# Kernel optimization log

Measured on AMD Instinct MI355X. Metric: run time of the kernel, lower is better.

The kernel has to match this reference:

```python
import jax, jax.numpy as jnp
import numpy as np

N_NODES = 50000
N_EDGES = 1_600_000
IN_DIM = 256
OUT_DIM = 128
NEG_SLOPE = 0.01  # F.leaky_relu default


def setup_inputs() -> dict:
    key = jax.random.key(0)
    k1, k2, k3, k4, k5 = jax.random.split(key, 5)
    x = jax.random.normal(k1, (N_NODES, IN_DIM), dtype=jnp.float32)
    # glorot_init: uniform in [-r, r], r = sqrt(6/(in+out))
    r = np.sqrt(6.0 / (IN_DIM + OUT_DIM)).astype(np.float32)
    weight = jax.random.uniform(k2, (IN_DIM, OUT_DIM), dtype=jnp.float32, minval=-r, maxval=r)
    adj_rows = jax.random.randint(k3, (N_EDGES,), 0, N_NODES, dtype=jnp.int64 if jax.config.jax_enable_x64 else jnp.int32)
    adj_cols = jax.random.randint(k4, (N_EDGES,), 0, N_NODES, dtype=jnp.int64 if jax.config.jax_enable_x64 else jnp.int32)
    adj_vals = jax.random.uniform(k5, (N_EDGES,), dtype=jnp.float32)
    return {"x": x, "weight": weight, "adj_vals": adj_vals,
            "adj_rows": adj_rows, "adj_cols": adj_cols}


def reference(x, weight, adj_vals, adj_rows, adj_cols):
    # h = X @ W : [N, OUT_DIM]
    h = x @ weight
    # sparse adj @ h via edge-list SpMM: out[r] += v * h[c]
    msgs = adj_vals[:, None] * h[adj_cols]            # [E, OUT_DIM]
    agg = jax.ops.segment_sum(msgs, adj_rows, num_segments=N_NODES)
    # leaky_relu epilogue
    return jnp.where(agg >= 0, agg, NEG_SLOPE * agg)
```

## Files before the change

kernel.cpp:

```cpp
#include <hip/hip_runtime.h>
#include <hip/hip_fp16.h>

#define N_NODES 50000
#define N_EDGES 1600000
#define IN_DIM 256
#define OUT_DIM 128
#define NEG_SLOPE 0.01f

#define BIN_SH    5
#define BIN_ROWS  32
#define NBIN      ((N_NODES + BIN_ROWS - 1) / BIN_ROWS)
#define CAPB      1280
#define OVF_CAP   65536

#define SCAT_BLOCKS 256
#define CONVW_BLOCKS 8
#define EPB_S (N_EDGES / SCAT_BLOCKS)
#define SCAT_ITERS ((EPB_S + 511) / 512)

typedef _Float16 f16x8 __attribute__((ext_vector_type(8)));
typedef float    f32x4 __attribute__((ext_vector_type(4)));
typedef float    f32x8 __attribute__((ext_vector_type(8)));

__device__ __forceinline__ float lrelu(float v) {
    return v >= 0.f ? v : NEG_SLOPE * v;
}

#define BM 128
#define GEMM_BLOCKS ((N_NODES + BM - 1) / BM)

#define CVT16(lo, hi) do { \
    lo[0]=(_Float16)xr[0].x; lo[1]=(_Float16)xr[0].y; lo[2]=(_Float16)xr[0].z; lo[3]=(_Float16)xr[0].w; \
    lo[4]=(_Float16)xr[1].x; lo[5]=(_Float16)xr[1].y; lo[6]=(_Float16)xr[1].z; lo[7]=(_Float16)xr[1].w; \
    hi[0]=(_Float16)xr[2].x; hi[1]=(_Float16)xr[2].y; hi[2]=(_Float16)xr[2].z; hi[3]=(_Float16)xr[2].w; \
    hi[4]=(_Float16)xr[3].x; hi[5]=(_Float16)xr[3].y; hi[6]=(_Float16)xr[3].z; hi[7]=(_Float16)xr[3].w; \
} while (0)

__global__ __launch_bounds__(256, 2) void gemm_xw_mfma(const float* __restrict__ x,
                                                       const __half* __restrict__ wtl,
                                                       __half* __restrict__ h) {
    __shared__ f16x8 wt8[32 * 128];
    __shared__ f16x8 xs8[2][4][BM];

    const int t    = threadIdx.x;
    const int lane = t & 63;
    const int wv   = t >> 6;
    const int row0 = blockIdx.x * BM;

    {
        const int4* src = (const int4*)wtl;
        int4* dst = (int4*)wt8;
#pragma unroll
        for (int i = 0; i < 16; ++i) dst[i * 256 + t] = src[i * 256 + t];
    }

    const int srow = t >> 1;
    const int skh  = t & 1;
    const int grow = row0 + srow;
    const bool rv  = grow < N_NODES;
    const float* xp = x + (size_t)(rv ? grow : 0) * IN_DIM + skh * 16;

    float4 xr[4];
#pragma unroll
    for (int i = 0; i < 4; ++i)
        xr[i] = rv ? ((const float4*)xp)[i] : make_float4(0.f, 0.f, 0.f, 0.f);
    {
        f16x8 lo, hi;
        CVT16(lo, hi);
        xs8[0][skh * 2 + 0][srow] = lo;
        xs8[0][skh * 2 + 1][srow] = hi;
    }
    __syncthreads();

    f32x4 acc[2][8];
#pragma unroll
    for (int mf = 0; mf < 2; ++mf)
#pragma unroll
        for (int nf = 0; nf < 8; ++nf) acc[mf][nf] = (f32x4){0.f, 0.f, 0.f, 0.f};

    const int kg  = lane >> 4;
    const int l15 = lane & 15;
    const int mb  = (wv << 5) + l15;

#pragma unroll
    for (int ks = 0; ks < 8; ++ks) {
        const int cur = ks & 1;
        if (ks < 7) {
#pragma unroll
            for (int i = 0; i < 4; ++i)
                xr[i] = rv ? ((const float4*)(xp + (ks + 1) * 32))[i]
                           : make_float4(0.f, 0.f, 0.f, 0.f);
        }
        const f16x8 b0 = xs8[cur][kg][mb];
        const f16x8 b1 = xs8[cur][kg][mb + 16];
#pragma unroll
        for (int nf = 0; nf < 8; ++nf) {
            const f16x8 a = wt8[(((ks << 2) | kg) << 7) + (nf << 4) + l15];
            acc[0][nf] = __builtin_amdgcn_mfma_f32_16x16x32_f16(a, b0, acc[0][nf], 0, 0, 0);
            acc[1][nf] = __builtin_amdgcn_mfma_f32_16x16x32_f16(a, b1, acc[1][nf], 0, 0, 0);
        }
        if (ks < 7) {
            f16x8 lo, hi;
            CVT16(lo, hi);
            xs8[cur ^ 1][skh * 2 + 0][srow] = lo;
            xs8[cur ^ 1][skh * 2 + 1][srow] = hi;
            __syncthreads();
        }
    }

    const int rg = lane >> 4;
#pragma unroll
    for (int mf = 0; mf < 2; ++mf) {
        const int m = row0 + (wv << 5) + (mf << 4) + l15;
        if (m < N_NODES) {
            __half* hp = h + (size_t)m * OUT_DIM + (rg << 2);
#pragma unroll
            for (int nf = 0; nf < 8; ++nf) {
                union { ushort4 u; __half f[4]; } o;
                o.f[0] = __float2half(acc[mf][nf][0]);
                o.f[1] = __float2half(acc[mf][nf][1]);
                o.f[2] = __float2half(acc[mf][nf][2]);
                o.f[3] = __float2half(acc[mf][nf][3]);
                *(ushort4*)(hp + (nf << 4)) = o.u;
            }
        }
    }
}

__global__ __launch_bounds__(512) void scatter_bins(const int* __restrict__ rows,
                                                    const int* __restrict__ cols,
                                                    const float* __restrict__ vals,
                                                    int* __restrict__ cursor,
                                                    int* __restrict__ ovfcnt,
                                                    int2* __restrict__ ebuf,
                                                    int2* __restrict__ ovfbuf,
                                                    const float* __restrict__ w,
                                                    __half* __restrict__ wtl) {
    if (blockIdx.x >= SCAT_BLOCKS) {
        const int e0 = ((blockIdx.x - SCAT_BLOCKS) * 512 + threadIdx.x) * 8;
        const int k  = e0 >> 7;
        const int n0 = e0 & 127;
        const float4 a = *(const float4*)(w + e0);
        const float4 b = *(const float4*)(w + e0 + 4);
        __half* dst = wtl + ((size_t)((k >> 3) * 128 + n0)) * 8 + (k & 7);
        dst[0]  = __float2half(a.x);
        dst[8]  = __float2half(a.y);
        dst[16] = __float2half(a.z);
        dst[24] = __float2half(a.w);
        dst[32] = __float2half(b.x);
        dst[40] = __float2half(b.y);
        dst[48] = __float2half(b.z);
        dst[56] = __float2half(b.w);
        return;
    }

    __shared__ int lcur[NBIN];
    const int t = threadIdx.x;
    const int ebase = blockIdx.x * EPB_S;

    for (int b = t; b < NBIN; b += 512) lcur[b] = 0;
    __syncthreads();

    int myr[SCAT_ITERS];
#pragma unroll
    for (int k = 0; k < SCAT_ITERS; ++k) {
        const int i = k * 512 + t;
        myr[k] = -1;
        if (i < EPB_S) {
            const int r = rows[ebase + i];
            myr[k] = r;
            atomicAdd(&lcur[r >> BIN_SH], 1);
        }
    }
    __syncthreads();

    for (int b = t; b < NBIN; b += 512) {
        const int c = lcur[b];
        lcur[b] = (c > 0) ? atomicAdd(&cursor[b], c) : 0;
    }
    __syncthreads();

#pragma unroll
    for (int k = 0; k < SCAT_ITERS; ++k) {
        const int i = k * 512 + t;
        if (i < EPB_S) {
            const int e = ebase + i;
            const int r = myr[k];
            const int bin = r >> BIN_SH;
            const int off = atomicAdd(&lcur[bin], 1);
            const int key = cols[e] | ((r & (BIN_ROWS - 1)) << 16);
            const int vb  = __float_as_int(vals[e]);
            if (off < CAPB) {
                ebuf[(size_t)bin * CAPB + off] = make_int2(key, vb);
            } else {
                const int p = atomicAdd(ovfcnt, 1);
                if (p < OVF_CAP) ovfbuf[p] = make_int2(key | (bin << 21), vb);
            }
        }
    }
}

__global__ __launch_bounds__(512) void sort_gather(const int* __restrict__ cursor,
                                                   const int* __restrict__ ovfcnt,
                                                   const int2* __restrict__ ebuf,
                                                   const int2* __restrict__ ovfbuf,
                                                   const __half* __restrict__ h,
                                                   float* __restrict__ out) {
    __shared__ int2 srec[CAPB];
    __shared__ int  hist[BIN_ROWS];
    __shared__ int  rowoff_l[BIN_ROWS + 1];

    const int t    = threadIdx.x;
    const int bin  = blockIdx.x;
    const int wv   = t >> 6;
    const int lane = t & 63;

    const int cnt_all = cursor[bin];
    const int cnt     = cnt_all < CAPB ? cnt_all : CAPB;
    const size_t base = (size_t)bin * CAPB;

    if (t < BIN_ROWS) hist[t] = 0;
    __syncthreads();

    for (int i = t; i < cnt; i += 512)
        atomicAdd(&hist[(ebuf[base + i].x >> 16) & (BIN_ROWS - 1)], 1);
    __syncthreads();

    if (t < BIN_ROWS) {
        const int v = hist[t];
        int s = v;
#pragma unroll
        for (int off = 1; off < BIN_ROWS; off <<= 1) {
            const int u = __shfl_up(s, off);
            if (t >= off) s += u;
        }
        rowoff_l[t + 1] = s;
        hist[t] = s - v;
        if (t == 0) rowoff_l[0] = 0;
    }
    __syncthreads();

    for (int i = t; i < cnt; i += 512) {
        const int2 r = ebuf[base + i];
        const int pos = atomicAdd(&hist[(r.x >> 16) & (BIN_ROWS - 1)], 1);
        srec[pos] = r;
    }
    __syncthreads();

    const int grp = lane >> 4;
    const int gl  = lane & 15;
    const int novf = (cnt_all > CAPB) ? *ovfcnt : 0;

    for (int p = 0; p < 2; ++p) {
        const int lr0 = (wv << 2) + 2 * p;
        const int lr1 = lr0 + 1;
        const int b0 = rowoff_l[lr0], e0 = rowoff_l[lr0 + 1];
        const int b1 = rowoff_l[lr1], e1 = rowoff_l[lr1 + 1];
        const int n0 = e0 - b0, n1 = e1 - b1;
        const int nmax = n0 > n1 ? n0 : n1;
        const int iters = (nmax + 3) >> 2;

        f32x8 a0 = (f32x8){0.f,0.f,0.f,0.f,0.f,0.f,0.f,0.f};
        f32x8 a1 = (f32x8){0.f,0.f,0.f,0.f,0.f,0.f,0.f,0.f};

        for (int it = 0; it < iters; ++it) {
            const int i0 = b0 + (it << 2) + grp;
            const int i1 = b1 + (it << 2) + grp;
            const bool v0i = i0 < e0;
            const bool v1i = i1 < e1;
            const int2 rA = srec[v0i ? i0 : 0];
            const int2 rB = srec[v1i ? i1 : 0];
            const float vA = v0i ? __int_as_float(rA.y) : 0.f;
            const float vB = v1i ? __int_as_float(rB.y) : 0.f;
            const f16x8 hA = *(const f16x8*)(h + (size_t)(rA.x & 0xFFFF) * OUT_DIM + (gl << 3));
            const f16x8 hB = *(const f16x8*)(h + (size_t)(rB.x & 0xFFFF) * OUT_DIM + (gl << 3));
#pragma unroll
            for (int j = 0; j < 8; ++j) {
                a0[j] += vA * (float)hA[j];
                a1[j] += vB * (float)hB[j];
            }
        }

        for (int e = 0; e < novf; ++e) {
            const int2 rec = ovfbuf[e];
            if ((rec.x >> 21) == bin && grp == 0) {
                const int lrow = (rec.x >> 16) & (BIN_ROWS - 1);
                if (lrow == lr0 || lrow == lr1) {
                    const float v = __int_as_float(rec.y);
                    const f16x8 hv = *(const f16x8*)(h + (size_t)(rec.x & 0xFFFF) * OUT_DIM + (gl << 3));
#pragma unroll
                    for (int j = 0; j < 8; ++j) {
                        if (lrow == lr0) a0[j] += v * (float)hv[j];
                        else             a1[j] += v * (float)hv[j];
                    }
                }
            }
        }

#pragma unroll
        for (int j = 0; j < 8; ++j) {
            float x0 = a0[j], x1 = a1[j];
            x0 += __shfl_xor(x0, 16); x0 += __shfl_xor(x0, 32);
            x1 += __shfl_xor(x1, 16); x1 += __shfl_xor(x1, 32);
            a0[j] = x0; a1[j] = x1;
        }

        const int lrow = (grp & 2) ? lr1 : lr0;
        const int grow = (bin << BIN_SH) + lrow;
        float q[4];
#pragma unroll
        for (int k = 0; k < 4; ++k) {
            const float lo = (grp & 2) ? a1[k]     : a0[k];
            const float hi = (grp & 2) ? a1[k + 4] : a0[k + 4];
            q[k] = lrelu((grp & 1) ? hi : lo);
        }
        if (grow < N_NODES) {
            float4 o = make_float4(q[0], q[1], q[2], q[3]);
            *(float4*)(out + (size_t)grow * OUT_DIM + (gl << 3) + ((grp & 1) << 2)) = o;
        }
    }
}

extern "C" void kernel_launch(void* const* d_in, const int* in_sizes, int n_in,
                              void* d_out, int out_size, void* d_ws, size_t ws_size,
                              hipStream_t stream) {
    const float* x    = (const float*)d_in[0];
    const float* w    = (const float*)d_in[1];
    const float* vals = (const float*)d_in[2];
    const int*   rows = (const int*)d_in[3];
    const int*   cols = (const int*)d_in[4];
    float* out = (float*)d_out;

    char* ws = (char*)d_ws;
    size_t off = 0;
    auto alloc = [&](size_t bytes) {
        void* p = ws + off;
        off = (off + bytes + 255) & ~(size_t)255;
        return p;
    };
    __half* h      = (__half*)alloc((size_t)N_NODES * OUT_DIM * sizeof(__half));
    int2*  ebuf    = (int2*) alloc((size_t)NBIN * CAPB * sizeof(int2));
    int2*  ovfbuf  = (int2*) alloc((size_t)OVF_CAP * sizeof(int2));
    __half* wtl    = (__half*)alloc((size_t)IN_DIM * OUT_DIM * sizeof(__half));
    int*   meta    = (int*)  alloc((size_t)(NBIN + 1) * sizeof(int));
    int*   cursor  = meta;
    int*   ovfcnt  = meta + NBIN;

    hipMemsetAsync(meta, 0, (size_t)(NBIN + 1) * sizeof(int), stream);

    scatter_bins<<<SCAT_BLOCKS + CONVW_BLOCKS, 512, 0, stream>>>(rows, cols, vals,
                                                                 cursor, ovfcnt, ebuf, ovfbuf, w, wtl);
    gemm_xw_mfma<<<GEMM_BLOCKS, 256, 0, stream>>>(x, wtl, h);
    sort_gather<<<NBIN, 512, 0, stream>>>(cursor, ovfcnt, ebuf, ovfbuf, h, out);
}
```

Measured before the change: 203.7 us.

## Split edge binning into coarse and fine radix passes, sub-sort rows by column

Edge scatter now runs as two passes. A coarse pass buckets edges into 1024-row superbins, so per-block shared counters and global atomics cover 49 bins instead of about 1563. A fine pass then redistributes each superbin into 32-row bins, which is meant to make the scattered writes more local and coalesced. sort_gather also sub-sorts each row's edges by column high bits, so gathers from h have better locality. The cost is an extra kernel launch and an extra read and write of all 1.6M edges through a staging buffer aliased with h. Every gather block now scans the global overflow list regardless of its own count.

After: 200.6 us. Within noise of the previous version (-1.5%).

```diff
diff --git a/kernel.cpp b/kernel.cpp
--- a/kernel.cpp
+++ b/kernel.cpp
@@ -7,9 +7,17 @@
 #define OUT_DIM 128
 #define NEG_SLOPE 0.01f
 
+#define SB_SH     10
+#define SB_ROWS   1024
+#define NSB       ((N_NODES + SB_ROWS - 1) / SB_ROWS)
+#define SB_CAP    34816
+#define PASSB_SPLIT 8
+#define PB_ITERS  ((SB_CAP / PASSB_SPLIT + 511) / 512)
+
 #define BIN_SH    5
 #define BIN_ROWS  32
 #define NBIN      ((N_NODES + BIN_ROWS - 1) / BIN_ROWS)
+#define NBIN_PAD  (NSB * (SB_ROWS / BIN_ROWS))
 #define CAPB      1280
 #define OVF_CAP   65536
 
@@ -127,15 +135,15 @@
     }
 }
 
-__global__ __launch_bounds__(512) void scatter_bins(const int* __restrict__ rows,
-                                                    const int* __restrict__ cols,
-                                                    const float* __restrict__ vals,
-                                                    int* __restrict__ cursor,
-                                                    int* __restrict__ ovfcnt,
-                                                    int2* __restrict__ ebuf,
-                                                    int2* __restrict__ ovfbuf,
-                                                    const float* __restrict__ w,
-                                                    __half* __restrict__ wtl) {
+__global__ __launch_bounds__(512) void scatter_coarse(const int* __restrict__ rows,
+                                                      const int* __restrict__ cols,
+                                                      const float* __restrict__ vals,
+                                                      int* __restrict__ sbcur,
+                                                      int* __restrict__ ovfcnt,
+                                                      int2* __restrict__ cbuf,
+                                                      int2* __restrict__ ovfbuf,
+                                                      const float* __restrict__ w,
+                                                      __half* __restrict__ wtl) {
     if (blockIdx.x >= SCAT_BLOCKS) {
         const int e0 = ((blockIdx.x - SCAT_BLOCKS) * 512 + threadIdx.x) * 8;
         const int k  = e0 >> 7;
@@ -154,11 +162,11 @@
         return;
     }
 
-    __shared__ int lcur[NBIN];
+    __shared__ int lcur[NSB];
     const int t = threadIdx.x;
     const int ebase = blockIdx.x * EPB_S;
 
-    for (int b = t; b < NBIN; b += 512) lcur[b] = 0;
+    if (t < NSB) lcur[t] = 0;
     __syncthreads();
 
     int myr[SCAT_ITERS];
@@ -169,14 +177,14 @@
         if (i < EPB_S) {
             const int r = rows[ebase + i];
             myr[k] = r;
-            atomicAdd(&lcur[r >> BIN_SH], 1);
-        }
-    }
-    __syncthreads();
-
-    for (int b = t; b < NBIN; b += 512) {
-        const int c = lcur[b];
-        lcur[b] = (c > 0) ? atomicAdd(&cursor[b], c) : 0;
+            atomicAdd(&lcur[r >> SB_SH], 1);
+        }
+    }
+    __syncthreads();
+
+    if (t < NSB) {
+        const int c = lcur[t];
+        lcur[t] = (c > 0) ? atomicAdd(&sbcur[t], c) : 0;
     }
     __syncthreads();
 
@@ -186,28 +194,86 @@
         if (i < EPB_S) {
             const int e = ebase + i;
             const int r = myr[k];
-            const int bin = r >> BIN_SH;
-            const int off = atomicAdd(&lcur[bin], 1);
-            const int key = cols[e] | ((r & (BIN_ROWS - 1)) << 16);
+            const int sb = r >> SB_SH;
+            const int off = atomicAdd(&lcur[sb], 1);
+            const int key = (int)(((unsigned)r << 16) | (unsigned)cols[e]);
             const int vb  = __float_as_int(vals[e]);
-            if (off < CAPB) {
-                ebuf[(size_t)bin * CAPB + off] = make_int2(key, vb);
+            if (off < SB_CAP) {
+                cbuf[(size_t)sb * SB_CAP + off] = make_int2(key, vb);
             } else {
                 const int p = atomicAdd(ovfcnt, 1);
-                if (p < OVF_CAP) ovfbuf[p] = make_int2(key | (bin << 21), vb);
+                if (p < OVF_CAP) ovfbuf[p] = make_int2(key, vb);
             }
         }
     }
 }
 
-__global__ __launch_bounds__(512) void sort_gather(const int* __restrict__ cursor,
+__global__ __launch_bounds__(512) void scatter_fine(const int* __restrict__ sbcur,
+                                                    int* __restrict__ fcur,
+                                                    int* __restrict__ ovfcnt,
+                                                    const int2* __restrict__ cbuf,
+                                                    int2* __restrict__ ebuf,
+                                                    int2* __restrict__ ovfbuf) {
+    __shared__ int lcur[SB_ROWS / BIN_ROWS];
+    const int t    = threadIdx.x;
+    const int sb   = blockIdx.x / PASSB_SPLIT;
+    const int part = blockIdx.x % PASSB_SPLIT;
+
+    const int cnt_sb = min(sbcur[sb], SB_CAP);
+    const int chunk  = (cnt_sb + PASSB_SPLIT - 1) / PASSB_SPLIT;
+    const int i0 = part * chunk;
+    const int i1 = min(i0 + chunk, cnt_sb);
+
+    if (t < 32) lcur[t] = 0;
+    __syncthreads();
+
+    int2 rc[PB_ITERS];
+#pragma unroll
+    for (int k = 0; k < PB_ITERS; ++k) {
+        const int i = i0 + k * 512 + t;
+        if (i < i1) {
+            rc[k] = cbuf[(size_t)sb * SB_CAP + i];
+            const unsigned urow = ((unsigned)rc[k].x) >> 16;
+            atomicAdd(&lcur[(urow >> BIN_SH) & 31], 1);
+        }
+    }
+    __syncthreads();
+
+    if (t < 32) {
+        const int c = lcur[t];
+        lcur[t] = (c > 0) ? atomicAdd(&fcur[(sb << 5) + t], c) : 0;
+    }
+    __syncthreads();
+
+#pragma unroll
+    for (int k = 0; k < PB_ITERS; ++k) {
+        const int i = i0 + k * 512 + t;
+        if (i < i1) {
+            const unsigned urow = ((unsigned)rc[k].x) >> 16;
+            const int f   = (int)(urow >> BIN_SH);
+            const int off = atomicAdd(&lcur[(urow >> BIN_SH) & 31], 1);
+            const int key = (rc[k].x & 0xFFFF) | (int)((urow & (BIN_ROWS - 1)) << 16);
+            if (off < CAPB) {
+                ebuf[(size_t)f * CAPB + off] = make_int2(key, rc[k].y);
+            } else {
+                const int p = atomicAdd(ovfcnt, 1);
+                if (p < OVF_CAP) ovfbuf[p] = rc[k];
+            }
+        }
+    }
+}
+
+#define NCLS 256
+
+__global__ __launch_bounds__(512) void sort_gather(const int* __restrict__ fcur,
                                                    const int* __restrict__ ovfcnt,
                                                    const int2* __restrict__ ebuf,
                                                    const int2* __restrict__ ovfbuf,
                                                    const __half* __restrict__ h,
                                                    float* __restrict__ out) {
     __shared__ int2 srec[CAPB];
-    __shared__ int  hist[BIN_ROWS];
+    __shared__ int  hist[NCLS];
+    __shared__ int  pfx[NCLS];
     __shared__ int  rowoff_l[BIN_ROWS + 1];
 
     const int t    = threadIdx.x;
@@ -215,41 +281,44 @@
     const int wv   = t >> 6;
     const int lane = t & 63;
 
-    const int cnt_all = cursor[bin];
+    const int cnt_all = fcur[bin];
     const int cnt     = cnt_all < CAPB ? cnt_all : CAPB;
     const size_t base = (size_t)bin * CAPB;
 
-    if (t < BIN_ROWS) hist[t] = 0;
-    __syncthreads();
-
-    for (int i = t; i < cnt; i += 512)
-        atomicAdd(&hist[(ebuf[base + i].x >> 16) & (BIN_ROWS - 1)], 1);
-    __syncthreads();
-
-    if (t < BIN_ROWS) {
-        const int v = hist[t];
-        int s = v;
-#pragma unroll
-        for (int off = 1; off < BIN_ROWS; off <<= 1) {
-            const int u = __shfl_up(s, off);
-            if (t >= off) s += u;
-        }
-        rowoff_l[t + 1] = s;
-        hist[t] = s - v;
-        if (t == 0) rowoff_l[0] = 0;
-    }
+    if (t < NCLS) hist[t] = 0;
+    __syncthreads();
+
+    for (int i = t; i < cnt; i += 512) {
+        const int k = ebuf[base + i].x;
+        atomicAdd(&hist[(((k >> 16) & 31) << 3) | ((k & 0xFFFF) >> 13)], 1);
+    }
+    __syncthreads();
+
+    if (t < NCLS) pfx[t] = hist[t];
+    __syncthreads();
+    for (int off = 1; off < NCLS; off <<= 1) {
+        const int u = (t >= off && t < NCLS) ? pfx[t - off] : 0;
+        __syncthreads();
+        if (t < NCLS) pfx[t] += u;
+        __syncthreads();
+    }
+    if (t < NCLS) hist[t] = pfx[t] - hist[t];
+    if (t < BIN_ROWS) rowoff_l[t] = t ? pfx[(t << 3) - 1] : 0;
+    if (t == BIN_ROWS) rowoff_l[BIN_ROWS] = cnt;
     __syncthreads();
 
     for (int i = t; i < cnt; i += 512) {
         const int2 r = ebuf[base + i];
-        const int pos = atomicAdd(&hist[(r.x >> 16) & (BIN_ROWS - 1)], 1);
+        const int cls = (((r.x >> 16) & 31) << 3) | ((r.x & 0xFFFF) >> 13);
+        const int pos = atomicAdd(&hist[cls], 1);
         srec[pos] = r;
     }
     __syncthreads();
 
     const int grp = lane >> 4;
     const int gl  = lane & 15;
-    const int novf = (cnt_all > CAPB) ? *ovfcnt : 0;
+    int novf = *ovfcnt;
+    if (novf > OVF_CAP) novf = OVF_CAP;
 
     for (int p = 0; p < 2; ++p) {
         const int lr0 = (wv << 2) + 2 * p;
@@ -283,8 +352,9 @@
 
         for (int e = 0; e < novf; ++e) {
             const int2 rec = ovfbuf[e];
-            if ((rec.x >> 21) == bin && grp == 0) {
-                const int lrow = (rec.x >> 16) & (BIN_ROWS - 1);
+            const unsigned urow = ((unsigned)rec.x) >> 16;
+            if ((int)(urow >> BIN_SH) == bin && grp == 0) {
+                const int lrow = (int)(urow & (BIN_ROWS - 1));
                 if (lrow == lr0 || lrow == lr1) {
                     const float v = __int_as_float(rec.y);
                     const f16x8 hv = *(const f16x8*)(h + (size_t)(rec.x & 0xFFFF) * OUT_DIM + (gl << 3));
@@ -338,18 +408,21 @@
         off = (off + bytes + 255) & ~(size_t)255;
         return p;
     };
-    __half* h      = (__half*)alloc((size_t)N_NODES * OUT_DIM * sizeof(__half));
+    int2*  cbuf    = (int2*) alloc((size_t)NSB * SB_CAP * sizeof(int2));
+    __half* h      = (__half*)cbuf;
     int2*  ebuf    = (int2*) alloc((size_t)NBIN * CAPB * sizeof(int2));
     int2*  ovfbuf  = (int2*) alloc((size_t)OVF_CAP * sizeof(int2));
     __half* wtl    = (__half*)alloc((size_t)IN_DIM * OUT_DIM * sizeof(__half));
-    int*   meta    = (int*)  alloc((size_t)(NBIN + 1) * sizeof(int));
-    int*   cursor  = meta;
-    int*   ovfcnt  = meta + NBIN;
-
-    hipMemsetAsync(meta, 0, (size_t)(NBIN + 1) * sizeof(int), stream);
-
-    scatter_bins<<<SCAT_BLOCKS + CONVW_BLOCKS, 512, 0, stream>>>(rows, cols, vals,
-                                                                 cursor, ovfcnt, ebuf, ovfbuf, w, wtl);
+    int*   meta    = (int*)  alloc((size_t)(NSB + NBIN_PAD + 1) * sizeof(int));
+    int*   sbcur   = meta;
+    int*   fcur    = meta + NSB;
+    int*   ovfcnt  = meta + NSB + NBIN_PAD;
+
+    hipMemsetAsync(meta, 0, (size_t)(NSB + NBIN_PAD + 1) * sizeof(int), stream);
+
+    scatter_coarse<<<SCAT_BLOCKS + CONVW_BLOCKS, 512, 0, stream>>>(rows, cols, vals,
+                                                                   sbcur, ovfcnt, cbuf, ovfbuf, w, wtl);
+    scatter_fine<<<NSB * PASSB_SPLIT, 512, 0, stream>>>(sbcur, fcur, ovfcnt, cbuf, ebuf, ovfbuf);
     gemm_xw_mfma<<<GEMM_BLOCKS, 256, 0, stream>>>(x, wtl, h);
-    sort_gather<<<NBIN, 512, 0, stream>>>(cursor, ovfcnt, ebuf, ovfbuf, h, out);
-}
+    sort_gather<<<NBIN, 512, 0, stream>>>(fcur, ovfcnt, ebuf, ovfbuf, h, out);
+}
```
